# Performance work log

Measured on AMD Instinct MI355X. Metric: run time of the kernel, lower is better.

Reference implementation:

```python
import jax, jax.numpy as jnp
import numpy as np

IN_G, OUT_G, IN_MEM, OUT_MEM, N_EMBED = 64, 64, 8, 8, 512
DIM_QUANT = IN_MEM * OUT_MEM  # 64
B = 8192


def setup_inputs() -> dict:
    key = jax.random.key(0)
    k1, k2, k3 = jax.random.split(key, 3)
    x = jax.random.normal(k1, (B, IN_G * IN_MEM), dtype=jnp.float32)
    # xavier-uniform-ish init for weight
    bound = float(np.sqrt(6.0 / (IN_MEM + OUT_MEM)))
    weight = jax.random.uniform(k2, (IN_G, OUT_G, IN_MEM, OUT_MEM), dtype=jnp.float32,
                                minval=-bound, maxval=bound)
    # VQ codebook, stored (dim, n_embed) as in rosinality Quantize
    embed = jax.random.normal(k3, (DIM_QUANT, N_EMBED), dtype=jnp.float32)
    return {"x": x, "weight": weight, "embed": embed, "use_qw": 1}


def _quantize(w_flat, embed):
    # w_flat: [G, dim]; embed: [dim, n_embed]
    # dist = ||w||^2 - 2 w@e + ||e||^2  (squared euclidean)
    dist = ((w_flat ** 2).sum(axis=1, keepdims=True)
            - 2.0 * (w_flat @ embed)
            + (embed ** 2).sum(axis=0, keepdims=True))
    idx = jnp.argmin(dist, axis=1)
    quant = jnp.take(embed.T, idx, axis=0)  # embed_code: embedding on embed.T
    return quant, idx


def reference(x, weight, embed, use_qw):
    in_g, out_g, in_mem, out_mem = weight.shape
    b = x.shape[0]
    xg = x.reshape(b, in_g, in_mem).transpose(1, 0, 2)  # [g, b, i]
    if use_qw:
        w_flat = weight.reshape(in_g * out_g, in_mem * out_mem)
        quant, _ = _quantize(w_flat, embed)
        quant = quant.reshape(weight.shape)
        diff = jnp.mean((jax.lax.stop_gradient(quant) - weight) ** 2)
        # straight-through estimator
        q_w = weight + jax.lax.stop_gradient(quant - weight)
    else:
        q_w = weight
        diff = None
    # permute(0,2,1,3).reshape -> [g, in_mem, out_g*out_mem]
    q_w = q_w.transpose(0, 2, 1, 3).reshape(in_g, in_mem, out_g * out_mem)
    # grouped matmul + stack + sum over groups == single einsum contraction over g and i
    res = jnp.einsum('gbi,gio->bo', xg, q_w)  # [b, out_g*out_mem]
    return (res, diff)
```

## Files before the change

kernel.cpp:

```cpp
#include <hip/hip_runtime.h>
#include <cstdint>

#define NEMB   512
#define DQ     64
#define NROWS  4096
#define BATCH  8192
#define KDIM   512
#define NDIM   512

typedef __attribute__((ext_vector_type(8))) short bf16x8;
typedef __attribute__((ext_vector_type(4))) float floatx4;

__device__ __forceinline__ unsigned short f2bf(float f) {
    unsigned int u = __float_as_uint(f);
    u += 0x7fffu + ((u >> 16) & 1u);
    return (unsigned short)(u >> 16);
}

__device__ __forceinline__ void async16(const void* g, void* l) {
    __builtin_amdgcn_global_load_lds(
        (const __attribute__((address_space(1))) void*)g,
        (__attribute__((address_space(3))) void*)l, 16, 0, 0);
}

__global__ __launch_bounds__(256) void prep_kernel(
    const float* __restrict__ x,
    const float* __restrict__ embed,
    unsigned short* __restrict__ xb,
    double* __restrict__ e2,
    float* diff_slot)
{
    const int gid = blockIdx.x * 256 + threadIdx.x;
#pragma unroll
    for (int it = 0; it < 2; ++it) {
        const int idx = gid + it * 524288;
        float4 v = reinterpret_cast<const float4*>(x)[idx];
        ushort4 o;
        o.x = f2bf(v.x); o.y = f2bf(v.y); o.z = f2bf(v.z); o.w = f2bf(v.w);
        reinterpret_cast<ushort4*>(xb)[idx] = o;
    }
    if (gid < NEMB) {
        double s = 0.0;
        for (int d = 0; d < DQ; ++d) {
            double e = (double)embed[d * NEMB + gid];
            s = fma(e, e, s);
        }
        e2[gid] = s;
    }
    if (gid == 0 && diff_slot) *diff_slot = 0.f;
}

__global__ __launch_bounds__(256) void vq_kernel(
    const float* __restrict__ weight,
    const float* __restrict__ embed,
    const double* __restrict__ e2,
    unsigned short* __restrict__ wt,
    float* diff_out,
    const int* __restrict__ use_qw)
{
    const int t    = threadIdx.x;
    const int wave = t >> 6;
    const int lane = t & 63;
    const int rblk = blockIdx.x * 16;
    const bool qon = (use_qw[0] != 0);

    __shared__ float wlds[16 * 64];
    __shared__ int   bidx_lds[16];

    reinterpret_cast<float4*>(wlds)[t] =
        reinterpret_cast<const float4*>(weight + (size_t)rblk * 64)[t];
    __syncthreads();

    if (qon) {
        const int j0 = lane * 8;
        const int rw = wave * 4;

        double acc[4][8];
#pragma unroll
        for (int r = 0; r < 4; ++r)
#pragma unroll
            for (int c = 0; c < 8; ++c) acc[r][c] = 0.0;

        for (int d = 0; d < DQ; ++d) {
            const float4 ea = *reinterpret_cast<const float4*>(embed + d * NEMB + j0);
            const float4 eb = *reinterpret_cast<const float4*>(embed + d * NEMB + j0 + 4);
            double ev[8];
            ev[0] = (double)ea.x; ev[1] = (double)ea.y; ev[2] = (double)ea.z; ev[3] = (double)ea.w;
            ev[4] = (double)eb.x; ev[5] = (double)eb.y; ev[6] = (double)eb.z; ev[7] = (double)eb.w;
#pragma unroll
            for (int r = 0; r < 4; ++r) {
                const double wv = (double)wlds[(rw + r) * 64 + d];
#pragma unroll
                for (int c = 0; c < 8; ++c)
                    acc[r][c] = fma(wv, ev[c], acc[r][c]);
            }
        }

        double e2v[8];
#pragma unroll
        for (int c = 0; c < 8; ++c) e2v[c] = e2[j0 + c];

#pragma unroll
        for (int r = 0; r < 4; ++r) {
            double best = 1e300;
            int bi = 0;
#pragma unroll
            for (int c = 0; c < 8; ++c) {
                const double q = fma(-2.0, acc[r][c], e2v[c]);
                if (q < best) { best = q; bi = j0 + c; }
            }
#pragma unroll
            for (int off = 1; off < 64; off <<= 1) {
                const double ob = __shfl_xor(best, off, 64);
                const int    oi = __shfl_xor(bi,   off, 64);
                if (ob < best || (ob == best && oi < bi)) { best = ob; bi = oi; }
            }
            if (lane == 0) bidx_lds[rw + r] = bi;
        }
    }
    __syncthreads();

    const int sub  = t & 15;
    const int rloc = t >> 4;
    const int row  = rblk + rloc;
    const int g = row >> 6, og = row & 63;
    const int bidx = qon ? bidx_lds[rloc] : 0;
    const float* wr = wlds + rloc * 64;

    float dsum = 0.f;
#pragma unroll
    for (int z = 0; z < 4; ++z) {
        const int d = sub * 4 + z;
        const float wv = wr[d];
        float qv;
        if (qon) {
            qv = embed[d * NEMB + bidx];
            const float df = qv - wv;
            dsum = fmaf(df, df, dsum);
        } else {
            qv = wv;
        }
        const int i = d >> 3, om = d & 7;
        wt[(size_t)(og * 8 + om) * KDIM + (g * 8 + i)] = f2bf(qv);
    }

#pragma unroll
    for (int off = 32; off > 0; off >>= 1) dsum += __shfl_down(dsum, off, 64);
    __shared__ float red[4];
    if (lane == 0) red[wave] = dsum;
    __syncthreads();
    if (t == 0 && qon && diff_out)
        atomicAdd(diff_out, (red[0] + red[1] + red[2] + red[3]) * (1.f / (NROWS * DQ)));
}

__global__ __launch_bounds__(256) void gemm_kernel(
    const unsigned short* __restrict__ xb,
    const unsigned short* __restrict__ wt,
    float* __restrict__ out)
{
    __shared__ unsigned short As[128 * 32];
    __shared__ unsigned short Bs[64 * 32];

    const int tid  = threadIdx.x;
    const int wave = tid >> 6;
    const int lane = tid & 63;
    const int m0 = blockIdx.y * 128;
    const int n0 = blockIdx.x * 64;
    const int wm = (wave >> 1) * 64;
    const int wn = (wave & 1) * 32;

    const int srow = lane >> 2;
    const int scol = (lane & 3) * 8;
    const int mrow = lane & 15;
    const int koff = (lane >> 4) * 8;

    floatx4 acc[4][2] = {};

    for (int k0 = 0; k0 < KDIM; k0 += 32) {
        __syncthreads();
#pragma unroll
        for (int c = 0; c < 2; ++c) {
            const int q = wave * 2 + c;
            const int row = q * 16 + srow;
            async16(xb + (size_t)(m0 + row) * KDIM + k0 + scol, (char*)As + q * 1024);
        }
        {
            const int row = wave * 16 + srow;
            async16(wt + (size_t)(n0 + row) * KDIM + k0 + scol, (char*)Bs + wave * 1024);
        }
        __syncthreads();

        bf16x8 a[4], b[2];
#pragma unroll
        for (int i = 0; i < 4; ++i)
            a[i] = *reinterpret_cast<const bf16x8*>(&As[(wm + i * 16 + mrow) * 32 + koff]);
#pragma unroll
        for (int j = 0; j < 2; ++j)
            b[j] = *reinterpret_cast<const bf16x8*>(&Bs[(wn + j * 16 + mrow) * 32 + koff]);
#pragma unroll
        for (int i = 0; i < 4; ++i)
#pragma unroll
            for (int j = 0; j < 2; ++j)
                acc[i][j] = __builtin_amdgcn_mfma_f32_16x16x32_bf16(a[i], b[j], acc[i][j], 0, 0, 0);
    }

    const int col = lane & 15;
    const int rbase = (lane >> 4) * 4;
#pragma unroll
    for (int i = 0; i < 4; ++i)
#pragma unroll
        for (int j = 0; j < 2; ++j)
#pragma unroll
            for (int r = 0; r < 4; ++r) {
                const int mm = m0 + wm + i * 16 + rbase + r;
                const int nn = n0 + wn + j * 16 + col;
                out[(size_t)mm * NDIM + nn] = acc[i][j][r];
            }
}

extern "C" void kernel_launch(void* const* d_in, const int* in_sizes, int n_in,
                              void* d_out, int out_size, void* d_ws, size_t ws_size,
                              hipStream_t stream)
{
    const float* x      = (const float*)d_in[0];
    const float* weight = (const float*)d_in[1];
    const float* embed  = (const float*)d_in[2];
    const int*   use_qw = (const int*)d_in[3];
    float* out = (float*)d_out;

    unsigned short* wt = (unsigned short*)d_ws;
    double* e2         = (double*)((char*)d_ws + (512u << 10));
    unsigned short* xb = (unsigned short*)((char*)d_ws + (1u << 20));

    float* diff_slot = (out_size > BATCH * NDIM) ? (out + (size_t)BATCH * NDIM) : nullptr;

    prep_kernel<<<2048, 256, 0, stream>>>(x, embed, xb, e2, diff_slot);
    vq_kernel<<<NROWS / 16, 256, 0, stream>>>(weight, embed, e2, wt, diff_slot, use_qw);
    gemm_kernel<<<dim3(NDIM / 64, BATCH / 128), 256, 0, stream>>>(xb, wt, out);
}
```

Baseline: 113.3 us.

## Fuse prep and VQ kernels, shrink GEMM tile with XCD-aware block mapping

Merges the bf16 conversion of x and the VQ codebook search into one launch, computing codebook norms inline instead of in a separate pass. The atomic diff accumulation becomes per-block partial sums, which the GEMM kernel reduces at the end. Weight-table stores are vectorised to 16-byte writes. The GEMM moves to 64x64 tiles with a flat grid remapped per XCD and an occupancy hint, trading more A-tile reloads for more resident blocks and better L2 locality.

```diff
diff --git a/kernel.cpp b/kernel.cpp
--- a/kernel.cpp
+++ b/kernel.cpp
@@ -8,6 +8,9 @@
 #define KDIM   512
 #define NDIM   512
 
+#define CONV_BLOCKS 2048
+#define VQ_BLOCKS   256
+
 typedef __attribute__((ext_vector_type(8))) short bf16x8;
 typedef __attribute__((ext_vector_type(4))) float floatx4;
 
@@ -23,49 +26,40 @@
         (__attribute__((address_space(3))) void*)l, 16, 0, 0);
 }
 
-__global__ __launch_bounds__(256) void prep_kernel(
+__global__ __launch_bounds__(256) void fused_prep_vq(
     const float* __restrict__ x,
+    const float* __restrict__ weight,
     const float* __restrict__ embed,
     unsigned short* __restrict__ xb,
-    double* __restrict__ e2,
-    float* diff_slot)
-{
-    const int gid = blockIdx.x * 256 + threadIdx.x;
-#pragma unroll
-    for (int it = 0; it < 2; ++it) {
-        const int idx = gid + it * 524288;
-        float4 v = reinterpret_cast<const float4*>(x)[idx];
-        ushort4 o;
-        o.x = f2bf(v.x); o.y = f2bf(v.y); o.z = f2bf(v.z); o.w = f2bf(v.w);
-        reinterpret_cast<ushort4*>(xb)[idx] = o;
-    }
-    if (gid < NEMB) {
-        double s = 0.0;
-        for (int d = 0; d < DQ; ++d) {
-            double e = (double)embed[d * NEMB + gid];
-            s = fma(e, e, s);
-        }
-        e2[gid] = s;
-    }
-    if (gid == 0 && diff_slot) *diff_slot = 0.f;
-}
-
-__global__ __launch_bounds__(256) void vq_kernel(
-    const float* __restrict__ weight,
-    const float* __restrict__ embed,
-    const double* __restrict__ e2,
     unsigned short* __restrict__ wt,
-    float* diff_out,
+    float* __restrict__ partials,
     const int* __restrict__ use_qw)
 {
-    const int t    = threadIdx.x;
+    const int t   = threadIdx.x;
+    const int bid = blockIdx.x;
+
+    if (bid < CONV_BLOCKS) {
+        const int gid = bid * 256 + t;
+#pragma unroll
+        for (int it = 0; it < 2; ++it) {
+            const int idx = gid + it * 524288;
+            float4 v = reinterpret_cast<const float4*>(x)[idx];
+            ushort4 o;
+            o.x = f2bf(v.x); o.y = f2bf(v.y); o.z = f2bf(v.z); o.w = f2bf(v.w);
+            reinterpret_cast<ushort4*>(xb)[idx] = o;
+        }
+        return;
+    }
+
+    const int vb   = bid - CONV_BLOCKS;
     const int wave = t >> 6;
     const int lane = t & 63;
-    const int rblk = blockIdx.x * 16;
+    const int rblk = vb * 16;
     const bool qon = (use_qw[0] != 0);
 
     __shared__ float wlds[16 * 64];
     __shared__ int   bidx_lds[16];
+    __shared__ float red[4];
 
     reinterpret_cast<float4*>(wlds)[t] =
         reinterpret_cast<const float4*>(weight + (size_t)rblk * 64)[t];
@@ -76,6 +70,9 @@
         const int rw = wave * 4;
 
         double acc[4][8];
+        double ee[8];
+#pragma unroll
+        for (int c = 0; c < 8; ++c) ee[c] = 0.0;
 #pragma unroll
         for (int r = 0; r < 4; ++r)
 #pragma unroll
@@ -88,6 +85,8 @@
             ev[0] = (double)ea.x; ev[1] = (double)ea.y; ev[2] = (double)ea.z; ev[3] = (double)ea.w;
             ev[4] = (double)eb.x; ev[5] = (double)eb.y; ev[6] = (double)eb.z; ev[7] = (double)eb.w;
 #pragma unroll
+            for (int c = 0; c < 8; ++c) ee[c] = fma(ev[c], ev[c], ee[c]);
+#pragma unroll
             for (int r = 0; r < 4; ++r) {
                 const double wv = (double)wlds[(rw + r) * 64 + d];
 #pragma unroll
@@ -95,10 +94,6 @@
                     acc[r][c] = fma(wv, ev[c], acc[r][c]);
             }
         }
-
-        double e2v[8];
-#pragma unroll
-        for (int c = 0; c < 8; ++c) e2v[c] = e2[j0 + c];
 
 #pragma unroll
         for (int r = 0; r < 4; ++r) {
@@ -106,7 +101,7 @@
             int bi = 0;
 #pragma unroll
             for (int c = 0; c < 8; ++c) {
-                const double q = fma(-2.0, acc[r][c], e2v[c]);
+                const double q = fma(-2.0, acc[r][c], ee[c]);
                 if (q < best) { best = q; bi = j0 + c; }
             }
 #pragma unroll
@@ -120,53 +115,60 @@
     }
     __syncthreads();
 
-    const int sub  = t & 15;
-    const int rloc = t >> 4;
-    const int row  = rblk + rloc;
-    const int g = row >> 6, og = row & 63;
-    const int bidx = qon ? bidx_lds[rloc] : 0;
-    const float* wr = wlds + rloc * 64;
-
     float dsum = 0.f;
-#pragma unroll
-    for (int z = 0; z < 4; ++z) {
-        const int d = sub * 4 + z;
-        const float wv = wr[d];
-        float qv;
-        if (qon) {
-            qv = embed[d * NEMB + bidx];
-            const float df = qv - wv;
-            dsum = fmaf(df, df, dsum);
-        } else {
-            qv = wv;
-        }
-        const int i = d >> 3, om = d & 7;
-        wt[(size_t)(og * 8 + om) * KDIM + (g * 8 + i)] = f2bf(qv);
+    if (t < 128) {
+        const int rloc = t >> 3, om = t & 7;
+        const int row = rblk + rloc;
+        const int g = row >> 6, og = row & 63;
+        const int bidx = qon ? bidx_lds[rloc] : 0;
+        alignas(16) unsigned short q8[8];
+#pragma unroll
+        for (int i = 0; i < 8; ++i) {
+            const int d = i * 8 + om;
+            const float wv = wlds[rloc * 64 + d];
+            float qv;
+            if (qon) {
+                qv = embed[d * NEMB + bidx];
+                const float df = qv - wv;
+                dsum = fmaf(df, df, dsum);
+            } else {
+                qv = wv;
+            }
+            q8[i] = f2bf(qv);
+        }
+        *reinterpret_cast<int4*>(wt + (size_t)(og * 8 + om) * KDIM + g * 8) =
+            *reinterpret_cast<const int4*>(q8);
     }
 
 #pragma unroll
     for (int off = 32; off > 0; off >>= 1) dsum += __shfl_down(dsum, off, 64);
-    __shared__ float red[4];
     if (lane == 0) red[wave] = dsum;
     __syncthreads();
-    if (t == 0 && qon && diff_out)
-        atomicAdd(diff_out, (red[0] + red[1] + red[2] + red[3]) * (1.f / (NROWS * DQ)));
-}
-
-__global__ __launch_bounds__(256) void gemm_kernel(
+    if (t == 0) partials[vb] = red[0] + red[1] + red[2] + red[3];
+}
+
+__global__ __launch_bounds__(256, 4) void gemm_kernel(
     const unsigned short* __restrict__ xb,
     const unsigned short* __restrict__ wt,
-    float* __restrict__ out)
+    float* __restrict__ out,
+    const float* __restrict__ partials,
+    float* diff_slot)
 {
-    __shared__ unsigned short As[128 * 32];
+    __shared__ unsigned short As[64 * 32];
     __shared__ unsigned short Bs[64 * 32];
 
     const int tid  = threadIdx.x;
     const int wave = tid >> 6;
     const int lane = tid & 63;
-    const int m0 = blockIdx.y * 128;
-    const int n0 = blockIdx.x * 64;
-    const int wm = (wave >> 1) * 64;
+
+    const int flat = blockIdx.x;
+    const int xcd  = flat & 7;
+    const int idx  = flat >> 3;
+    const int mt   = xcd * 16 + (idx >> 3);
+    const int nt   = idx & 7;
+    const int m0 = mt * 64;
+    const int n0 = nt * 64;
+    const int wm = (wave >> 1) * 32;
     const int wn = (wave & 1) * 32;
 
     const int srow = lane >> 2;
@@ -174,31 +176,26 @@
     const int mrow = lane & 15;
     const int koff = (lane >> 4) * 8;
 
-    floatx4 acc[4][2] = {};
+    floatx4 acc[2][2] = {};
 
     for (int k0 = 0; k0 < KDIM; k0 += 32) {
         __syncthreads();
-#pragma unroll
-        for (int c = 0; c < 2; ++c) {
-            const int q = wave * 2 + c;
-            const int row = q * 16 + srow;
-            async16(xb + (size_t)(m0 + row) * KDIM + k0 + scol, (char*)As + q * 1024);
-        }
         {
             const int row = wave * 16 + srow;
+            async16(xb + (size_t)(m0 + row) * KDIM + k0 + scol, (char*)As + wave * 1024);
             async16(wt + (size_t)(n0 + row) * KDIM + k0 + scol, (char*)Bs + wave * 1024);
         }
         __syncthreads();
 
-        bf16x8 a[4], b[2];
-#pragma unroll
-        for (int i = 0; i < 4; ++i)
+        bf16x8 a[2], b[2];
+#pragma unroll
+        for (int i = 0; i < 2; ++i)
             a[i] = *reinterpret_cast<const bf16x8*>(&As[(wm + i * 16 + mrow) * 32 + koff]);
 #pragma unroll
         for (int j = 0; j < 2; ++j)
             b[j] = *reinterpret_cast<const bf16x8*>(&Bs[(wn + j * 16 + mrow) * 32 + koff]);
 #pragma unroll
-        for (int i = 0; i < 4; ++i)
+        for (int i = 0; i < 2; ++i)
 #pragma unroll
             for (int j = 0; j < 2; ++j)
                 acc[i][j] = __builtin_amdgcn_mfma_f32_16x16x32_bf16(a[i], b[j], acc[i][j], 0, 0, 0);
@@ -207,7 +204,7 @@
     const int col = lane & 15;
     const int rbase = (lane >> 4) * 4;
 #pragma unroll
-    for (int i = 0; i < 4; ++i)
+    for (int i = 0; i < 2; ++i)
 #pragma unroll
         for (int j = 0; j < 2; ++j)
 #pragma unroll
@@ -216,6 +213,14 @@
                 const int nn = n0 + wn + j * 16 + col;
                 out[(size_t)mm * NDIM + nn] = acc[i][j][r];
             }
+
+    if (flat == 0 && wave == 0 && diff_slot) {
+        float s = partials[lane] + partials[lane + 64]
+                + partials[lane + 128] + partials[lane + 192];
+#pragma unroll
+        for (int off = 32; off > 0; off >>= 1) s += __shfl_down(s, off, 64);
+        if (lane == 0) diff_slot[0] = s * (1.f / (NROWS * DQ));
+    }
 }
 
 extern "C" void kernel_launch(void* const* d_in, const int* in_sizes, int n_in,
@@ -228,13 +233,13 @@
     const int*   use_qw = (const int*)d_in[3];
     float* out = (float*)d_out;
 
-    unsigned short* wt = (unsigned short*)d_ws;
-    double* e2         = (double*)((char*)d_ws + (512u << 10));
-    unsigned short* xb = (unsigned short*)((char*)d_ws + (1u << 20));
+    unsigned short* wt   = (unsigned short*)d_ws;
+    float* partials      = (float*)((char*)d_ws + (512u << 10));
+    unsigned short* xb   = (unsigned short*)((char*)d_ws + (1u << 20));
 
     float* diff_slot = (out_size > BATCH * NDIM) ? (out + (size_t)BATCH * NDIM) : nullptr;
 
-    prep_kernel<<<2048, 256, 0, stream>>>(x, embed, xb, e2, diff_slot);
-    vq_kernel<<<NROWS / 16, 256, 0, stream>>>(weight, embed, e2, wt, diff_slot, use_qw);
-    gemm_kernel<<<dim3(NDIM / 64, BATCH / 128), 256, 0, stream>>>(xb, wt, out);
-}
+    fused_prep_vq<<<CONV_BLOCKS + VQ_BLOCKS, 256, 0, stream>>>(
+        x, weight, embed, xb, wt, partials, use_qw);
+    gemm_kernel<<<1024, 256, 0, stream>>>(xb, wt, out, partials, diff_slot);
+}
```

Measured after the change: 122.1 us. 1.08x slower.
